# Kernel tuning notes

Measured on AMD Instinct MI355X. Metric: run time of the kernel, lower is better.

Reference implementation:

```python
import jax, jax.numpy as jnp
import numpy as np

N_NODES, N_EDGES = 10000, 160000
LATENT, N_EXP, N_SPECIES = 128, 8, 16
AVG_NEIGH = 16.0
EPS = 1e-8
# irreps: 64x0e + 32x1e + 16x2e -> flat dim 64 + 32*3 + 16*5 = 240

def _split(x):
    return x[:, :64], x[:, 64:160].reshape(-1, 32, 3), x[:, 160:240].reshape(-1, 16, 5)

def _merge(s, v, t):
    return jnp.concatenate([s, v.reshape(v.shape[0], -1), t.reshape(t.shape[0], -1)], axis=-1)

def _sep_ln(x, g, b):
    # separable layer norm: LN on scalars, per-degree component RMS norm on l>0
    s, v, t = _split(x)
    s = (s - s.mean(-1, keepdims=True)) * jax.lax.rsqrt(s.var(-1, keepdims=True) + EPS) * g[:64] + b
    v = v * jax.lax.rsqrt((v * v).mean((1, 2), keepdims=True) + EPS) * g[64:96][None, :, None]
    t = t * jax.lax.rsqrt((t * t).mean((1, 2), keepdims=True) + EPS) * g[96:112][None, :, None]
    return _merge(s, v, t)

def _forward(latents, node_features, edge_features, node_onehot, edge_vector,
             ln_gn, ln_bn, ln_ge, ln_be, Wg, W0, W1, W2, P0, b0, P1, P2,
             Wenv, benv, T0, T1, T2, edge_index):
    ec, en = edge_index[0], edge_index[1]
    nf_n = _sep_ln(node_features, ln_gn, ln_bn)
    ef_n = _sep_ln(edge_features, ln_ge, ln_be)
    # gather center/neighbor node features per edge (irregular access)
    c0, c1, c2 = _split(nf_n[ec])
    n0, n1, n2 = _split(nf_n[en])
    e0, e1, e2 = _split(ef_n)
    in0 = jnp.concatenate([c0, e0, n0], -1)   # [E,192]
    in1 = jnp.concatenate([c1, e1, n1], 1)    # [E,96,3]
    in2 = jnp.concatenate([c2, e2, n2], 1)    # [E,48,5]
    # latent-conditioned MoE tensor product: per-l linear with expert-mixed weights
    gates = jax.nn.softmax(latents @ Wg, axis=-1)            # [E,K]
    out0 = jnp.einsum('ek,kio,ei->eo', gates, W0, in0)        # [E,112]
    out1 = jnp.einsum('ek,kio,eim->eom', gates, W1, in1)      # [E,32,3]
    out2 = jnp.einsum('ek,kio,eim->eom', gates, W2, in2)      # [E,16,5]
    # gated nonlinearity: silu scalars, sigmoid gates multiply l>0 blocks
    s = jax.nn.silu(out0[:, :64])
    g1 = jax.nn.sigmoid(out0[:, 64:96])
    g2 = jax.nn.sigmoid(out0[:, 96:112])
    v = out1 * g1[:, :, None]
    t = out2 * g2[:, :, None]
    # lin_post (per-degree linear, bias on scalars)
    s = s @ P0 + b0
    v = jnp.einsum('eim,io->eom', v, P1)
    t = jnp.einsum('eim,io->eom', t, P2)
    # env element-wise weighting from latents (E3ElementLinear)
    w = latents @ Wenv + benv                                 # [E,112]
    msg = _merge(s * w[:, :64], v * w[:, 64:96, None], t * w[:, 96:112, None])
    # scatter-aggregate to center nodes
    agg = jax.ops.segment_sum(msg, ec, num_segments=node_features.shape[0])
    new_nf = agg * (AVG_NEIGH ** -0.5)
    # residual update with logit-parametrized ratio (param=0 -> u=0.5)
    u = jax.nn.sigmoid(jnp.zeros((), new_nf.dtype))
    c_old = jax.lax.rsqrt(u * u + 1.0)
    c_new = u * c_old
    nf = c_old * node_features + c_new * new_nf
    # species one-hot fully-connected TP correction
    s2, v2, t2 = _split(nf)
    ds = jnp.einsum('ni,nk,iko->no', s2, node_onehot, T0)
    dv = jnp.einsum('nim,nk,iko->nom', v2, node_onehot, T1)
    dt = jnp.einsum('nim,nk,iko->nom', t2, node_onehot, T2)
    return nf + _merge(ds, dv, dt)

def setup_inputs():
    key = jax.random.key(0)
    ks = jax.random.split(key, 20)
    f32 = jnp.float32
    return {
        'latents': jax.random.normal(ks[0], (N_EDGES, LATENT), f32),
        'node_features': jax.random.normal(ks[1], (N_NODES, 240), f32),
        'edge_features': jax.random.normal(ks[2], (N_EDGES, 240), f32),
        'node_onehot': jax.nn.one_hot(jax.random.randint(ks[3], (N_NODES,), 0, N_SPECIES), N_SPECIES, dtype=f32),
        'edge_vector': jax.random.normal(ks[4], (N_EDGES, 3), f32),
        'ln_gn': jnp.ones((112,), f32), 'ln_bn': jnp.zeros((64,), f32),
        'ln_ge': jnp.ones((112,), f32), 'ln_be': jnp.zeros((64,), f32),
        'Wg': jax.random.normal(ks[5], (LATENT, N_EXP), f32) * 0.1,
        'W0': jax.random.normal(ks[6], (N_EXP, 192, 112), f32) / float(np.sqrt(192)),
        'W1': jax.random.normal(ks[7], (N_EXP, 96, 32), f32) / float(np.sqrt(96)),
        'W2': jax.random.normal(ks[8], (N_EXP, 48, 16), f32) / float(np.sqrt(48)),
        'P0': jax.random.normal(ks[9], (64, 64), f32) / 8.0,
        'b0': jnp.zeros((64,), f32),
        'P1': jax.random.normal(ks[10], (32, 32), f32) / float(np.sqrt(32)),
        'P2': jax.random.normal(ks[11], (16, 16), f32) / 4.0,
        'Wenv': jax.random.normal(ks[12], (LATENT, 112), f32) / float(np.sqrt(LATENT)),
        'benv': jnp.zeros((112,), f32),
        'T0': jax.random.normal(ks[13], (64, N_SPECIES, 64), f32) / float(np.sqrt(64 * N_SPECIES)),
        'T1': jax.random.normal(ks[14], (32, N_SPECIES, 32), f32) / float(np.sqrt(32 * N_SPECIES)),
        'T2': jax.random.normal(ks[15], (16, N_SPECIES, 16), f32) / float(np.sqrt(16 * N_SPECIES)),
        'edge_index': jax.random.randint(ks[16], (2, N_EDGES), 0, N_NODES),
    }

def reference(latents, node_features, edge_features, node_onehot, edge_vector,
              ln_gn, ln_bn, ln_ge, ln_be, Wg, W0, W1, W2, P0, b0, P1, P2,
              Wenv, benv, T0, T1, T2, edge_index):
    return _forward(latents, node_features, edge_features, node_onehot, edge_vector,
                    ln_gn, ln_bn, ln_ge, ln_be, Wg, W0, W1, W2, P0, b0, P1, P2,
                    Wenv, benv, T0, T1, T2, edge_index)
```

## Files before the change

kernel.cpp:

```cpp
#include <hip/hip_runtime.h>
#include <math.h>

#define N_NODES 10000
#define N_EDGES 160000
#define EPS 1e-8f

typedef __attribute__((ext_vector_type(8))) __bf16 bf16x8;
typedef __attribute__((ext_vector_type(4))) float f32x4;

__device__ __forceinline__ f32x4 MFMA(bf16x8 a, bf16x8 b, f32x4 c){
  return __builtin_amdgcn_mfma_f32_16x16x32_bf16(a, b, c, 0, 0, 0);
}

__device__ __forceinline__ float wave_sum64(float x) {
  #pragma unroll
  for (int m = 32; m >= 1; m >>= 1) x += __shfl_xor(x, m, 64);
  return x;
}
__device__ __forceinline__ float gsum16(float x) {
  x += __shfl_xor(x, 1, 64); x += __shfl_xor(x, 2, 64);
  x += __shfl_xor(x, 4, 64); x += __shfl_xor(x, 8, 64);
  return x;
}

#define X0O 0
#define X1O 6400
#define X2O 16384
#define WvO 27904
#define O0O 0
#define O1O 6400
#define O2O 16384
#define SMEM_BYTES 64640

#define W0O 0
#define W1O 196608
#define W2O 221184
#define WEO 229376
#define P0O 245760
#define P1O 249856
#define P2O 250880
#define WTOT 251392

__device__ __forceinline__ void prep_seg(int u, const float* __restrict__ src,
                                         __bf16* __restrict__ dst,
                                         int NT, int KS, int Ka, int Na) {
  int per = NT * KS * 512;
  int e = u / per; int r = u - e * per;
  int nt = r / (KS * 512); r -= nt * KS * 512;
  int ks = r >> 9; int li = r & 511;
  int lane = li >> 3, j = li & 7;
  int k = ks * 32 + ((lane >> 4) << 3) + j;
  int n = nt * 16 + (lane & 15);
  float v = (k < Ka && n < Na) ? src[((size_t)e * Ka + k) * Na + n] : 0.f;
  dst[u] = (__bf16)v;
}

__global__ __launch_bounds__(256)
void k_prep(const float* __restrict__ W0, const float* __restrict__ W1,
            const float* __restrict__ W2, const float* __restrict__ We,
            const float* __restrict__ P0, const float* __restrict__ P1,
            const float* __restrict__ P2, __bf16* __restrict__ dst) {
  int t = blockIdx.x * 256 + threadIdx.x;
  if (t >= WTOT) return;
  if      (t < W1O) prep_seg(t - W0O, W0, dst + W0O, 8, 6, 192, 112);
  else if (t < W2O) prep_seg(t - W1O, W1, dst + W1O, 2, 3,  96,  32);
  else if (t < WEO) prep_seg(t - W2O, W2, dst + W2O, 1, 2,  48,  16);
  else if (t < P0O) prep_seg(t - WEO, We, dst + WEO, 8, 4, 128, 112);
  else if (t < P1O) prep_seg(t - P0O, P0, dst + P0O, 4, 2,  64,  64);
  else if (t < P2O) prep_seg(t - P1O, P1, dst + P1O, 2, 1,  32,  32);
  else              prep_seg(t - P2O, P2, dst + P2O, 1, 1,  16,  16);
}

__global__ __launch_bounds__(256)
void k_node_ln(const float* __restrict__ nf, const float* __restrict__ gn,
               const float* __restrict__ bn, __bf16* __restrict__ nfn) {
  int node = blockIdx.x * 4 + (threadIdx.x >> 6);
  int lane = threadIdx.x & 63;
  const float* row = nf + (size_t)node * 240;
  __bf16* out = nfn + (size_t)node * 240;
  float s = row[lane];
  float mean = wave_sum64(s) * (1.f / 64.f);
  float d = s - mean;
  float var = wave_sum64(d * d) * (1.f / 64.f);
  float rstd = rsqrtf(var + EPS);
  out[lane] = (__bf16)(d * rstd * gn[lane] + bn[lane]);
  float v0 = row[64 + lane];
  float v1 = (lane < 32) ? row[128 + lane] : 0.f;
  float rsv = rsqrtf(wave_sum64(v0 * v0 + v1 * v1) * (1.f / 96.f) + EPS);
  { int vi = lane; int i = vi / 3, m = vi - 3 * i;
    out[64 + m * 32 + i] = (__bf16)(v0 * rsv * gn[64 + i]); }
  if (lane < 32) { int vi = 64 + lane; int i = vi / 3, m = vi - 3 * i;
    out[64 + m * 32 + i] = (__bf16)(v1 * rsv * gn[64 + i]); }
  float t0 = row[160 + lane];
  float t1 = (lane < 16) ? row[224 + lane] : 0.f;
  float rst = rsqrtf(wave_sum64(t0 * t0 + t1 * t1) * (1.f / 80.f) + EPS);
  { int ti = lane; int i = ti / 5, m = ti - 5 * i;
    out[160 + m * 16 + i] = (__bf16)(t0 * rst * gn[96 + i]); }
  if (lane < 16) { int ti = 64 + lane; int i = ti / 5, m = ti - 5 * i;
    out[160 + m * 16 + i] = (__bf16)(t1 * rst * gn[96 + i]); }
}

__global__ __launch_bounds__(512, 4)
void k_edge(const float* __restrict__ latents, const float* __restrict__ ef,
            const __bf16* __restrict__ nfn, const int* __restrict__ eidx,
            const float* __restrict__ ln_ge, const float* __restrict__ ln_be,
            const float* __restrict__ Wg, const __bf16* __restrict__ Wsw,
            const float* __restrict__ pb0, const float* __restrict__ benv,
            float* __restrict__ agg) {
  __shared__ __align__(16) char smem[SMEM_BYTES];
  __bf16* SB = (__bf16*)smem;
  float* gatesL = (float*)(smem + 63488);
  int* ecsL = (int*)(smem + 64512);

  const int tid = threadIdx.x;
  const int e0 = blockIdx.x * 32;
  const int w = tid >> 6, lane = tid & 63, kg = lane >> 4, l16 = lane & 15;
  const int eg = tid >> 4, sl = tid & 15;

  const int ec = eidx[e0 + eg], en = eidx[N_EDGES + e0 + eg];
  if (tid < 32) ecsL[tid] = eidx[e0 + tid];
  uint2 cvr[4], nvr[4];
  #pragma unroll
  for (int j = 0; j < 4; ++j) {
    int ch = j * 16 + sl;
    if (ch < 60) {
      int p = ch * 4;
      cvr[j] = *(const uint2*)(nfn + (size_t)ec * 240 + p);
      nvr[j] = *(const uint2*)(nfn + (size_t)en * 240 + p);
    }
  }

  {
    const int mt = w >> 2, np = (w & 3) * 2;
    f32x4 acc[2] = {};
    const __bf16* WB = Wsw + WEO;
    #pragma unroll
    for (int ks = 0; ks < 4; ++ks) {
      bf16x8 a;
      const float* lp = latents + (size_t)(e0 + mt * 16 + l16) * 128 + ks * 32 + kg * 8;
      float4 u4 = *(const float4*)lp; float4 v4 = *(const float4*)(lp + 4);
      a[0]=(__bf16)u4.x; a[1]=(__bf16)u4.y; a[2]=(__bf16)u4.z; a[3]=(__bf16)u4.w;
      a[4]=(__bf16)v4.x; a[5]=(__bf16)v4.y; a[6]=(__bf16)v4.z; a[7]=(__bf16)v4.w;
      bf16x8 bA = *(const bf16x8*)(WB + ((np * 4 + ks) << 9) + lane * 8);
      bf16x8 bB = *(const bf16x8*)(WB + (((np + 1) * 4 + ks) << 9) + lane * 8);
      acc[0] = MFMA(a, bA, acc[0]); acc[1] = MFMA(a, bB, acc[1]);
    }
    #pragma unroll
    for (int ni = 0; ni < 2; ++ni) {
      int cc = (np + ni) * 16 + l16;
      if (cc < 112) {
        float bv = benv[cc];
        #pragma unroll
        for (int jj = 0; jj < 4; ++jj)
          SB[WvO + (mt * 16 + kg * 4 + jj) * 120 + cc] = (__bf16)(acc[ni][jj] + bv);
      }
    }
  }

  {
    #pragma unroll
    for (int j = 0; j < 4; ++j) {
      int ch = j * 16 + sl;
      if (ch < 60) {
        int p = ch * 4, dst, eoff;
        if (p < 64)       { dst = X0O + eg * 200 + p; eoff = 64; }
        else if (p < 160) { int q = p - 64; int m = q >> 5, i = q & 31;
                            dst = X1O + (m * 32 + eg) * 104 + i; eoff = 32; }
        else              { int q = p - 160; int m = q >> 4, i = q & 15;
                            dst = X2O + (m * 32 + eg) * 72 + i; eoff = 16; }
        *(uint2*)(SB + dst) = cvr[j];
        *(uint2*)(SB + dst + 2 * eoff) = nvr[j];
      }
    }
    for (int z = tid; z < 160 * 4; z += 512) {
      uint2 zz; zz.x = 0; zz.y = 0;
      *(uint2*)(SB + X2O + (z >> 2) * 72 + 48 + (z & 3) * 4) = zz;
    }

    const float* erow = ef + (size_t)(e0 + eg) * 240;
    float ev[15];
    #pragma unroll
    for (int j = 0; j < 15; ++j) ev[j] = erow[j * 16 + sl];
    float ssum = 0.f;
    #pragma unroll
    for (int j = 0; j < 4; ++j) ssum += ev[j];
    float mean = gsum16(ssum) * (1.f / 64.f);
    float sv = 0.f;
    #pragma unroll
    for (int j = 0; j < 4; ++j) { float dd = ev[j] - mean; sv += dd * dd; }
    float rstd = rsqrtf(gsum16(sv) * (1.f / 64.f) + EPS);
    float v2 = 0.f;
    #pragma unroll
    for (int j = 4; j < 10; ++j) v2 += ev[j] * ev[j];
    float rsv = rsqrtf(gsum16(v2) * (1.f / 96.f) + EPS);
    float t2 = 0.f;
    #pragma unroll
    for (int j = 10; j < 15; ++j) t2 += ev[j] * ev[j];
    float rst = rsqrtf(gsum16(t2) * (1.f / 80.f) + EPS);
    #pragma unroll
    for (int j = 0; j < 15; ++j) {
      const int c = j * 16 + sl;
      float x = ev[j], y; int eo;
      if (j < 4)       { y = (x - mean) * rstd * ln_ge[c] + ln_be[c];
                         eo = X0O + eg * 200 + 64 + c; }
      else if (j < 10) { int cc = c - 64; int i = cc / 3, m = cc - 3 * i;
                         y = x * rsv * ln_ge[64 + i];
                         eo = X1O + (m * 32 + eg) * 104 + 32 + i; }
      else             { int cc = c - 160; int i = cc / 5, m = cc - 5 * i;
                         y = x * rst * ln_ge[96 + i];
                         eo = X2O + (m * 32 + eg) * 72 + 16 + i; }
      SB[eo] = (__bf16)y;
    }

    const float* lrow = latents + (size_t)(e0 + eg) * 128 + sl * 8;
    float4 u4 = *(const float4*)lrow;
    float4 w4 = *(const float4*)(lrow + 4);
    float lv[8] = {u4.x, u4.y, u4.z, u4.w, w4.x, w4.y, w4.z, w4.w};
    float ga[8] = {};
    #pragma unroll
    for (int dd = 0; dd < 8; ++dd) {
      const float* wgr = Wg + (sl * 8 + dd) * 8;
      #pragma unroll
      for (int k = 0; k < 8; ++k) ga[k] += lv[dd] * wgr[k];
    }
    #pragma unroll
    for (int k = 0; k < 8; ++k) ga[k] = gsum16(ga[k]);
    float mx = ga[0];
    #pragma unroll
    for (int k = 1; k < 8; ++k) mx = fmaxf(mx, ga[k]);
    float den = 0.f;
    #pragma unroll
    for (int k = 0; k < 8; ++k) { ga[k] = expf(ga[k] - mx); den += ga[k]; }
    float val = 0.f;
    #pragma unroll
    for (int k = 0; k < 8; ++k) if (sl == k) val = ga[k];
    if (sl < 8) gatesL[eg * 8 + sl] = val / den;
  }
  __syncthreads();

  {
    const int mt = w & 1, ntA = (w >> 1) * 2;
    f32x4 acc[2] = {};
    const __bf16* WB = Wsw + W0O;
    for (int ex = 0; ex < 8; ++ex) {
      f32x4 D[2] = {};
      #pragma unroll
      for (int ks = 0; ks < 6; ++ks) {
        bf16x8 a = *(const bf16x8*)(SB + X0O + (mt * 16 + l16) * 200 + ks * 32 + kg * 8);
        bf16x8 bA = *(const bf16x8*)(WB + (((ex * 8 + ntA) * 6 + ks) << 9) + lane * 8);
        bf16x8 bB = *(const bf16x8*)(WB + (((ex * 8 + ntA + 1) * 6 + ks) << 9) + lane * 8);
        D[0] = MFMA(a, bA, D[0]); D[1] = MFMA(a, bB, D[1]);
      }
      #pragma unroll
      for (int jj = 0; jj < 4; ++jj) {
        float g = gatesL[(mt * 16 + kg * 4 + jj) * 8 + ex];
        acc[0][jj] += g * D[0][jj]; acc[1][jj] += g * D[1][jj];
      }
    }
    __syncthreads();
    #pragma unroll
    for (int ni = 0; ni < 2; ++ni) {
      int cc = (ntA + ni) * 16 + l16;
      if (cc < 112)
        #pragma unroll
        for (int jj = 0; jj < 4; ++jj) {
          float x = acc[ni][jj];
          float sg = 1.f / (1.f + expf(-x));
          float val = (cc < 64) ? x * sg : sg;
          SB[O0O + (mt * 16 + kg * 4 + jj) * 120 + cc] = (__bf16)val;
        }
    }
  }

  const int nu1 = (w < 4) ? 2 : 1;
  const int mtv0 = w >> 1, ntv = w & 1, mtv1 = (w >> 1) + 4;
  {
    f32x4 acc[2] = {};
    const __bf16* WB = Wsw + W1O;
    for (int ex = 0; ex < 8; ++ex) {
      f32x4 D[2] = {};
      #pragma unroll
      for (int ks = 0; ks < 3; ++ks) {
        bf16x8 b = *(const bf16x8*)(WB + (((ex * 2 + ntv) * 3 + ks) << 9) + lane * 8);
        bf16x8 a0 = *(const bf16x8*)(SB + X1O + (mtv0 * 16 + l16) * 104 + ks * 32 + kg * 8);
        D[0] = MFMA(a0, b, D[0]);
        if (nu1 == 2) {
          bf16x8 a1 = *(const bf16x8*)(SB + X1O + (mtv1 * 16 + l16) * 104 + ks * 32 + kg * 8);
          D[1] = MFMA(a1, b, D[1]);
        }
      }
      #pragma unroll
      for (int jj = 0; jj < 4; ++jj) {
        int r0 = mtv0 * 16 + kg * 4 + jj;
        acc[0][jj] += gatesL[(r0 & 31) * 8 + ex] * D[0][jj];
        if (nu1 == 2) {
          int r1 = mtv1 * 16 + kg * 4 + jj;
          acc[1][jj] += gatesL[(r1 & 31) * 8 + ex] * D[1][jj];
        }
      }
    }
    __syncthreads();
    const int o = ntv * 16 + l16;
    #pragma unroll
    for (int jj = 0; jj < 4; ++jj) {
      int r0 = mtv0 * 16 + kg * 4 + jj;
      float g0 = (float)SB[O0O + (r0 & 31) * 120 + 64 + o];
      SB[O1O + r0 * 40 + o] = (__bf16)(acc[0][jj] * g0);
      if (nu1 == 2) {
        int r1 = mtv1 * 16 + kg * 4 + jj;
        float g1 = (float)SB[O0O + (r1 & 31) * 120 + 64 + o];
        SB[O1O + r1 * 40 + o] = (__bf16)(acc[1][jj] * g1);
      }
    }
  }

  const int nu2 = (w < 2) ? 2 : 1;
  const int mt20 = w, mt21 = w + 8;
  {
    f32x4 acc[2] = {};
    const __bf16* WB = Wsw + W2O;
    for (int ex = 0; ex < 8; ++ex) {
      f32x4 D[2] = {};
      #pragma unroll
      for (int ks = 0; ks < 2; ++ks) {
        bf16x8 b = *(const bf16x8*)(WB + ((ex * 2 + ks) << 9) + lane * 8);
        bf16x8 a0 = *(const bf16x8*)(SB + X2O + (mt20 * 16 + l16) * 72 + ks * 32 + kg * 8);
        D[0] = MFMA(a0, b, D[0]);
        if (nu2 == 2) {
          bf16x8 a1 = *(const bf16x8*)(SB + X2O + (mt21 * 16 + l16) * 72 + ks * 32 + kg * 8);
          D[1] = MFMA(a1, b, D[1]);
        }
      }
      #pragma unroll
      for (int jj = 0; jj < 4; ++jj) {
        int r0 = mt20 * 16 + kg * 4 + jj;
        acc[0][jj] += gatesL[(r0 & 31) * 8 + ex] * D[0][jj];
        if (nu2 == 2) {
          int r1 = mt21 * 16 + kg * 4 + jj;
          acc[1][jj] += gatesL[(r1 & 31) * 8 + ex] * D[1][jj];
        }
      }
    }
    __syncthreads();
    #pragma unroll
    for (int jj = 0; jj < 4; ++jj) {
      int r0 = mt20 * 16 + kg * 4 + jj;
      float g0 = (float)SB[O0O + (r0 & 31) * 120 + 96 + l16];
      SB[O2O + r0 * 40 + l16] = (__bf16)(acc[0][jj] * g0);
      SB[O2O + r0 * 40 + 16 + l16] = (__bf16)0.f;
      if (nu2 == 2) {
        int r1 = mt21 * 16 + kg * 4 + jj;
        float g1 = (float)SB[O0O + (r1 & 31) * 120 + 96 + l16];
        SB[O2O + r1 * 40 + l16] = (__bf16)(acc[1][jj] * g1);
        SB[O2O + r1 * 40 + 16 + l16] = (__bf16)0.f;
      }
    }
  }
  __syncthreads();

  {
    const int mt = w & 1, nt = w >> 1;
    f32x4 ps = {};
    const __bf16* WB = Wsw + P0O;
    #pragma unroll
    for (int ks = 0; ks < 2; ++ks) {
      bf16x8 a = *(const bf16x8*)(SB + O0O + (mt * 16 + l16) * 120 + ks * 32 + kg * 8);
      bf16x8 b = *(const bf16x8*)(WB + ((nt * 2 + ks) << 9) + lane * 8);
      ps = MFMA(a, b, ps);
    }
    int cc = nt * 16 + l16;
    float bias = pb0[cc];
    #pragma unroll
    for (int jj = 0; jj < 4; ++jj) {
      int row = mt * 16 + kg * 4 + jj;
      float msg = (ps[jj] + bias) * (float)SB[WvO + row * 120 + cc];
      atomicAdd(&agg[(size_t)ecsL[row] * 240 + cc], msg);
    }
  }
  {
    f32x4 pv[2] = {};
    const __bf16* WB = Wsw + P1O;
    bf16x8 b = *(const bf16x8*)(WB + (ntv << 9) + lane * 8);
    bf16x8 a0 = *(const bf16x8*)(SB + O1O + (mtv0 * 16 + l16) * 40 + kg * 8);
    pv[0] = MFMA(a0, b, pv[0]);
    if (nu1 == 2) {
      bf16x8 a1 = *(const bf16x8*)(SB + O1O + (mtv1 * 16 + l16) * 40 + kg * 8);
      pv[1] = MFMA(a1, b, pv[1]);
    }
    const int o = ntv * 16 + l16;
    #pragma unroll
    for (int jj = 0; jj < 4; ++jj) {
      int r0 = mtv0 * 16 + kg * 4 + jj;
      int m = r0 >> 5, eL = r0 & 31;
      float msg = pv[0][jj] * (float)SB[WvO + eL * 120 + 64 + o];
      atomicAdd(&agg[(size_t)ecsL[eL] * 240 + 64 + m * 32 + o], msg);
      if (nu1 == 2) {
        int r1 = mtv1 * 16 + kg * 4 + jj;
        int m1 = r1 >> 5, eL1 = r1 & 31;
        float msg1 = pv[1][jj] * (float)SB[WvO + eL1 * 120 + 64 + o];
        atomicAdd(&agg[(size_t)ecsL[eL1] * 240 + 64 + m1 * 32 + o], msg1);
      }
    }
  }
  {
    f32x4 pt[2] = {};
    const __bf16* WB = Wsw + P2O;
    bf16x8 b = *(const bf16x8*)(WB + lane * 8);
    bf16x8 a0 = *(const bf16x8*)(SB + O2O + (mt20 * 16 + l16) * 40 + kg * 8);
    pt[0] = MFMA(a0, b, pt[0]);
    if (nu2 == 2) {
      bf16x8 a1 = *(const bf16x8*)(SB + O2O + (mt21 * 16 + l16) * 40 + kg * 8);
      pt[1] = MFMA(a1, b, pt[1]);
    }
    const int o = l16;
    #pragma unroll
    for (int jj = 0; jj < 4; ++jj) {
      int r0 = mt20 * 16 + kg * 4 + jj;
      int m = r0 >> 5, eL = r0 & 31;
      float msg = pt[0][jj] * (float)SB[WvO + eL * 120 + 96 + o];
      atomicAdd(&agg[(size_t)ecsL[eL] * 240 + 160 + m * 16 + o], msg);
      if (nu2 == 2) {
        int r1 = mt21 * 16 + kg * 4 + jj;
        int m1 = r1 >> 5, eL1 = r1 & 31;
        float msg1 = pt[1][jj] * (float)SB[WvO + eL1 * 120 + 96 + o];
        atomicAdd(&agg[(size_t)ecsL[eL1] * 240 + 160 + m1 * 16 + o], msg1);
      }
    }
  }
}

__global__ __launch_bounds__(256)
void k_node(const float* __restrict__ nf, const float* __restrict__ agg,
            const float* __restrict__ onehot, const float* __restrict__ T0,
            const float* __restrict__ T1, const float* __restrict__ T2,
            float* __restrict__ out) {
  int w = threadIdx.x >> 6;
  int lane = threadIdx.x & 63;
  int node = blockIdx.x * 4 + w;
  __shared__ float buf[4][240];
  const float* nrow = nf + (size_t)node * 240;
  const float* arow = agg + (size_t)node * 240;
  const float c_old = 0.894427190999916f;
  const float c_new_s = 0.447213595499958f * 0.25f;
  for (int j = lane; j < 240; j += 64) {
    int src;
    if (j < 64) src = j;
    else if (j < 160) { int vi = j - 64; int o = vi / 3, m = vi - 3 * o; src = 64 + m * 32 + o; }
    else              { int ti = j - 160; int o = ti / 5, m = ti - 5 * o; src = 160 + m * 16 + o; }
    buf[w][j] = c_old * nrow[j] + c_new_s * arow[src];
  }
  float ohv = (lane < 16) ? onehot[(size_t)node * 16 + lane] : 0.f;
  unsigned long long msk = __ballot(ohv > 0.5f);
  int kk = __ffsll((unsigned long long)msk) - 1;
  __syncthreads();
  #pragma unroll
  for (int rep = 0; rep < 4; ++rep) {
    int c = rep * 64 + lane;
    if (c >= 240) break;
    float d;
    if (c < 64) {
      const float* tp = T0 + (size_t)kk * 64 + c;
      float a = 0.f;
      for (int i = 0; i < 64; ++i) a = fmaf(buf[w][i], tp[(size_t)i * 1024], a);
      d = a;
    } else if (c < 160) {
      int vi = c - 64; int o = vi / 3, m = vi - o * 3;
      const float* tp = T1 + (size_t)kk * 32 + o;
      float a = 0.f;
      for (int i = 0; i < 32; ++i) a = fmaf(buf[w][64 + i * 3 + m], tp[(size_t)i * 512], a);
      d = a;
    } else {
      int ti = c - 160; int o = ti / 5, m = ti - o * 5;
      const float* tp = T2 + (size_t)kk * 16 + o;
      float a = 0.f;
      for (int i = 0; i < 16; ++i) a = fmaf(buf[w][160 + i * 5 + m], tp[(size_t)i * 256], a);
      d = a;
    }
    out[(size_t)node * 240 + c] = buf[w][c] + d;
  }
}

extern "C" void kernel_launch(void* const* d_in, const int* in_sizes, int n_in,
                              void* d_out, int out_size, void* d_ws, size_t ws_size,
                              hipStream_t stream) {
  (void)in_sizes; (void)n_in; (void)out_size; (void)ws_size;
  const float* latents       = (const float*)d_in[0];
  const float* node_features = (const float*)d_in[1];
  const float* edge_features = (const float*)d_in[2];
  const float* node_onehot   = (const float*)d_in[3];
  const float* ln_gn = (const float*)d_in[5];
  const float* ln_bn = (const float*)d_in[6];
  const float* ln_ge = (const float*)d_in[7];
  const float* ln_be = (const float*)d_in[8];
  const float* Wg    = (const float*)d_in[9];
  const float* W0    = (const float*)d_in[10];
  const float* W1    = (const float*)d_in[11];
  const float* W2    = (const float*)d_in[12];
  const float* P0    = (const float*)d_in[13];
  const float* b0    = (const float*)d_in[14];
  const float* P1    = (const float*)d_in[15];
  const float* P2    = (const float*)d_in[16];
  const float* Wenv  = (const float*)d_in[17];
  const float* benv  = (const float*)d_in[18];
  const float* T0    = (const float*)d_in[19];
  const float* T1    = (const float*)d_in[20];
  const float* T2    = (const float*)d_in[21];
  const int*   eidx  = (const int*)d_in[22];
  float* out = (float*)d_out;

  __bf16* nfn = (__bf16*)d_ws;
  float* agg = (float*)((char*)d_ws + 4800000);
  __bf16* Wsw = (__bf16*)((char*)d_ws + 14400000);

  hipMemsetAsync(agg, 0, 2400000 * sizeof(float), stream);
  k_prep<<<(WTOT + 255) / 256, 256, 0, stream>>>(W0, W1, W2, Wenv, P0, P1, P2, Wsw);
  k_node_ln<<<N_NODES / 4, 256, 0, stream>>>(node_features, ln_gn, ln_bn, nfn);
  k_edge<<<N_EDGES / 32, 512, 0, stream>>>(latents, edge_features, nfn, eidx,
      ln_ge, ln_be, Wg, Wsw, b0, benv, agg);
  k_node<<<N_NODES / 4, 256, 0, stream>>>(node_features, agg, node_onehot, T0, T1, T2, out);
}
```

Measured before the change: 436.9 us.

## Split edge LN stats and gating into pre-kernels, shrink and swizzle edge LDS

```diff
diff --git a/kernel.cpp b/kernel.cpp
--- a/kernel.cpp
+++ b/kernel.cpp
@@ -24,13 +24,13 @@
 }
 
 #define X0O 0
-#define X1O 6400
-#define X2O 16384
-#define WvO 27904
+#define X1O 6144
+#define X2O 15360
 #define O0O 0
-#define O1O 6400
-#define O2O 16384
-#define SMEM_BYTES 64640
+#define O1O 6144
+#define O2O 15360
+#define WvO 21760
+#define SMEM_BYTES 52352
 
 #define W0O 0
 #define W1O 196608
@@ -100,26 +100,79 @@
     out[160 + m * 16 + i] = (__bf16)(t1 * rst * gn[96 + i]); }
 }
 
-__global__ __launch_bounds__(512, 4)
+__global__ __launch_bounds__(256)
+void k_stats(const float* __restrict__ ef, float4* __restrict__ stats) {
+  int row = blockIdx.x * 4 + (threadIdx.x >> 6);
+  int lane = threadIdx.x & 63;
+  const float* r = ef + (size_t)row * 240;
+  float s = r[lane];
+  float mean = wave_sum64(s) * (1.f / 64.f);
+  float d = s - mean;
+  float var = wave_sum64(d * d) * (1.f / 64.f);
+  float rstd = rsqrtf(var + EPS);
+  float v0 = r[64 + lane];
+  float v1 = (lane < 32) ? r[128 + lane] : 0.f;
+  float rsv = rsqrtf(wave_sum64(v0 * v0 + v1 * v1) * (1.f / 96.f) + EPS);
+  float t0 = r[160 + lane];
+  float t1 = (lane < 16) ? r[224 + lane] : 0.f;
+  float rst = rsqrtf(wave_sum64(t0 * t0 + t1 * t1) * (1.f / 80.f) + EPS);
+  if (lane == 0) stats[row] = make_float4(mean, rstd, rsv, rst);
+}
+
+__global__ __launch_bounds__(256)
+void k_gate(const float* __restrict__ latents, const float* __restrict__ Wg,
+            float* __restrict__ gatesG) {
+  int row = blockIdx.x * 16 + (threadIdx.x >> 4);
+  int sl = threadIdx.x & 15;
+  const float* lrow = latents + (size_t)row * 128 + sl * 8;
+  float4 u4 = *(const float4*)lrow;
+  float4 w4 = *(const float4*)(lrow + 4);
+  float lv[8] = {u4.x, u4.y, u4.z, u4.w, w4.x, w4.y, w4.z, w4.w};
+  float ga[8] = {};
+  #pragma unroll
+  for (int dd = 0; dd < 8; ++dd) {
+    const float* wgr = Wg + (sl * 8 + dd) * 8;
+    #pragma unroll
+    for (int k = 0; k < 8; ++k) ga[k] += lv[dd] * wgr[k];
+  }
+  #pragma unroll
+  for (int k = 0; k < 8; ++k) ga[k] = gsum16(ga[k]);
+  float mx = ga[0];
+  #pragma unroll
+  for (int k = 1; k < 8; ++k) mx = fmaxf(mx, ga[k]);
+  float den = 0.f;
+  #pragma unroll
+  for (int k = 0; k < 8; ++k) { ga[k] = expf(ga[k] - mx); den += ga[k]; }
+  float val = 0.f;
+  #pragma unroll
+  for (int k = 0; k < 8; ++k) if (sl == k) val = ga[k];
+  if (sl < 8) gatesG[(size_t)row * 8 + sl] = val / den;
+}
+
+__global__ __launch_bounds__(512, 6)
 void k_edge(const float* __restrict__ latents, const float* __restrict__ ef,
             const __bf16* __restrict__ nfn, const int* __restrict__ eidx,
             const float* __restrict__ ln_ge, const float* __restrict__ ln_be,
-            const float* __restrict__ Wg, const __bf16* __restrict__ Wsw,
+            const float4* __restrict__ stats, const float* __restrict__ gatesG,
+            const __bf16* __restrict__ Wsw,
             const float* __restrict__ pb0, const float* __restrict__ benv,
             float* __restrict__ agg) {
   __shared__ __align__(16) char smem[SMEM_BYTES];
-  __bf16* SB = (__bf16*)smem;
-  float* gatesL = (float*)(smem + 63488);
-  int* ecsL = (int*)(smem + 64512);
+  float* gatesL = (float*)(smem + 51200);
+  int* ecsL = (int*)(smem + 52224);
+  __bf16* SBF = (__bf16*)smem;
 
   const int tid = threadIdx.x;
   const int e0 = blockIdx.x * 32;
   const int w = tid >> 6, lane = tid & 63, kg = lane >> 4, l16 = lane & 15;
   const int eg = tid >> 4, sl = tid & 15;
+  const int xsw = (eg & 7) << 4;
+  const int xswr = (l16 & 7) << 4;
 
   const int ec = eidx[e0 + eg], en = eidx[N_EDGES + e0 + eg];
   if (tid < 32) ecsL[tid] = eidx[e0 + tid];
-  uint2 cvr[4], nvr[4];
+  if (tid < 256) gatesL[tid] = gatesG[(size_t)e0 * 8 + tid];
+  uint2 cvr[4], nvr[4]; float4 evf[4];
   #pragma unroll
   for (int j = 0; j < 4; ++j) {
     int ch = j * 16 + sl;
@@ -127,6 +180,180 @@
       int p = ch * 4;
       cvr[j] = *(const uint2*)(nfn + (size_t)ec * 240 + p);
       nvr[j] = *(const uint2*)(nfn + (size_t)en * 240 + p);
+      evf[j] = *(const float4*)(ef + (size_t)(e0 + eg) * 240 + p);
+    }
+  }
+  float4 st = stats[e0 + eg];
+
+  {
+    #pragma unroll
+    for (int j = 0; j < 4; ++j) {
+      int ch = j * 16 + sl;
+      if (ch < 60) {
+        int p = ch * 4;
+        float e4[4] = {evf[j].x, evf[j].y, evf[j].z, evf[j].w};
+        if (p < 64) {
+          int off = X0O + eg * 192;
+          *(uint2*)(smem + (((off + p) * 2) ^ xsw)) = cvr[j];
+          *(uint2*)(smem + (((off + 128 + p) * 2) ^ xsw)) = nvr[j];
+          __bf16 eb[4];
+          #pragma unroll
+          for (int t = 0; t < 4; ++t) {
+            int c = p + t;
+            eb[t] = (__bf16)((e4[t] - st.x) * st.y * ln_ge[c] + ln_be[c]);
+          }
+          *(uint2*)(smem + (((off + 64 + p) * 2) ^ xsw)) = *(uint2*)eb;
+        } else if (p < 160) {
+          int q = p - 64;
+          int m = q >> 5, i = q & 31;
+          int off = X1O + (m * 32 + eg) * 96;
+          *(uint2*)(smem + (((off + i) * 2) ^ xsw)) = cvr[j];
+          *(uint2*)(smem + (((off + 64 + i) * 2) ^ xsw)) = nvr[j];
+          #pragma unroll
+          for (int t = 0; t < 4; ++t) {
+            int k = q + t; int ei = k / 3, em = k - 3 * ei;
+            float y = e4[t] * st.z * ln_ge[64 + ei];
+            *(__bf16*)(smem + (((X1O + (em * 32 + eg) * 96 + 32 + ei) * 2) ^ xsw)) = (__bf16)y;
+          }
+        } else {
+          int q = p - 160;
+          int m = q >> 4, i = q & 15;
+          int off = X2O + (m * 32 + eg) * 64;
+          *(uint2*)(smem + (((off + i) * 2) ^ xsw)) = cvr[j];
+          *(uint2*)(smem + (((off + 32 + i) * 2) ^ xsw)) = nvr[j];
+          #pragma unroll
+          for (int t = 0; t < 4; ++t) {
+            int k = q + t; int ei = k / 5, em = k - 5 * ei;
+            float y = e4[t] * st.w * ln_ge[96 + ei];
+            *(__bf16*)(smem + (((X2O + (em * 32 + eg) * 64 + 16 + ei) * 2) ^ xsw)) = (__bf16)y;
+          }
+        }
+      }
+    }
+    for (int z = tid; z < 640; z += 512) {
+      int r = z >> 2, c4 = (z & 3) * 4;
+      uint2 zz; zz.x = 0; zz.y = 0;
+      *(uint2*)(smem + (((X2O + r * 64 + 48 + c4) * 2) ^ ((r & 7) << 4))) = zz;
+    }
+  }
+  __syncthreads();
+
+  {
+    const int mt = w & 1, ntA = (w >> 1) * 2;
+    f32x4 acc[2] = {};
+    const __bf16* WB = Wsw + W0O;
+    for (int ex = 0; ex < 8; ++ex) {
+      f32x4 D[2] = {};
+      #pragma unroll
+      for (int ks = 0; ks < 6; ++ks) {
+        bf16x8 a = *(const bf16x8*)(smem + (((X0O + (mt * 16 + l16) * 192 + ks * 32 + kg * 8) * 2) ^ xswr));
+        bf16x8 bA = *(const bf16x8*)(WB + (((ex * 8 + ntA) * 6 + ks) << 9) + lane * 8);
+        bf16x8 bB = *(const bf16x8*)(WB + (((ex * 8 + ntA + 1) * 6 + ks) << 9) + lane * 8);
+        D[0] = MFMA(a, bA, D[0]); D[1] = MFMA(a, bB, D[1]);
+      }
+      #pragma unroll
+      for (int jj = 0; jj < 4; ++jj) {
+        float g = gatesL[(mt * 16 + kg * 4 + jj) * 8 + ex];
+        acc[0][jj] += g * D[0][jj]; acc[1][jj] += g * D[1][jj];
+      }
+    }
+    __syncthreads();
+    #pragma unroll
+    for (int ni = 0; ni < 2; ++ni) {
+      int cc = (ntA + ni) * 16 + l16;
+      if (cc < 112)
+        #pragma unroll
+        for (int jj = 0; jj < 4; ++jj) {
+          float x = acc[ni][jj];
+          float sg = 1.f / (1.f + expf(-x));
+          float val = (cc < 64) ? x * sg : sg;
+          SBF[O0O + (mt * 16 + kg * 4 + jj) * 120 + cc] = (__bf16)val;
+        }
+    }
+  }
+
+  const int nu1 = (w < 4) ? 2 : 1;
+  const int mtv0 = w >> 1, ntv = w & 1, mtv1 = (w >> 1) + 4;
+  {
+    f32x4 acc[2] = {};
+    const __bf16* WB = Wsw + W1O;
+    for (int ex = 0; ex < 8; ++ex) {
+      f32x4 D[2] = {};
+      #pragma unroll
+      for (int ks = 0; ks < 3; ++ks) {
+        bf16x8 b = *(const bf16x8*)(WB + (((ex * 2 + ntv) * 3 + ks) << 9) + lane * 8);
+        bf16x8 a0 = *(const bf16x8*)(smem + (((X1O + (mtv0 * 16 + l16) * 96 + ks * 32 + kg * 8) * 2) ^ xswr));
+        D[0] = MFMA(a0, b, D[0]);
+        if (nu1 == 2) {
+          bf16x8 a1 = *(const bf16x8*)(smem + (((X1O + (mtv1 * 16 + l16) * 96 + ks * 32 + kg * 8) * 2) ^ xswr));
+          D[1] = MFMA(a1, b, D[1]);
+        }
+      }
+      #pragma unroll
+      for (int jj = 0; jj < 4; ++jj) {
+        int r0 = mtv0 * 16 + kg * 4 + jj;
+        acc[0][jj] += gatesL[(r0 & 31) * 8 + ex] * D[0][jj];
+        if (nu1 == 2) {
+          int r1 = mtv1 * 16 + kg * 4 + jj;
+          acc[1][jj] += gatesL[(r1 & 31) * 8 + ex] * D[1][jj];
+        }
+      }
+    }
+    __syncthreads();
+    const int o = ntv * 16 + l16;
+    #pragma unroll
+    for (int jj = 0; jj < 4; ++jj) {
+      int r0 = mtv0 * 16 + kg * 4 + jj;
+      float g0 = (float)SBF[O0O + (r0 & 31) * 120 + 64 + o];
+      SBF[O1O + r0 * 40 + o] = (__bf16)(acc[0][jj] * g0);
+      if (nu1 == 2) {
+        int r1 = mtv1 * 16 + kg * 4 + jj;
+        float g1 = (float)SBF[O0O + (r1 & 31) * 120 + 64 + o];
+        SBF[O1O + r1 * 40 + o] = (__bf16)(acc[1][jj] * g1);
+      }
+    }
+  }
+
+  const int nu2 = (w < 2) ? 2 : 1;
+  const int mt20 = w, mt21 = w + 8;
+  {
+    f32x4 acc[2] = {};
+    const __bf16* WB = Wsw + W2O;
+    for (int ex = 0; ex < 8; ++ex) {
+      f32x4 D[2] = {};
+      #pragma unroll
+      for (int ks = 0; ks < 2; ++ks) {
+        bf16x8 b = *(const bf16x8*)(WB + ((ex * 2 + ks) << 9) + lane * 8);
+        bf16x8 a0 = *(const bf16x8*)(smem + (((X2O + (mt20 * 16 + l16) * 64 + ks * 32 + kg * 8) * 2) ^ xswr));
+        D[0] = MFMA(a0, b, D[0]);
+        if (nu2 == 2) {
+          bf16x8 a1 = *(const bf16x8*)(smem + (((X2O + (mt21 * 16 + l16) * 64 + ks * 32 + kg * 8) * 2) ^ xswr));
+          D[1] = MFMA(a1, b, D[1]);
+        }
+      }
+      #pragma unroll
+      for (int jj = 0; jj < 4; ++jj) {
+        int r0 = mt20 * 16 + kg * 4 + jj;
+        acc[0][jj] += gatesL[(r0 & 31) * 8 + ex] * D[0][jj];
+        if (nu2 == 2) {
+          int r1 = mt21 * 16 + kg * 4 + jj;
+          acc[1][jj] += gatesL[(r1 & 31) * 8 + ex] * D[1][jj];
+        }
+      }
+    }
+    __syncthreads();
+    #pragma unroll
+    for (int jj = 0; jj < 4; ++jj) {
+      int r0 = mt20 * 16 + kg * 4 + jj;
+      float g0 = (float)SBF[O0O + (r0 & 31) * 120 + 96 + l16];
+      SBF[O2O + r0 * 40 + l16] = (__bf16)(acc[0][jj] * g0);
+      SBF[O2O + r0 * 40 + 16 + l16] = (__bf16)0.f;
+      if (nu2 == 2) {
+        int r1 = mt21 * 16 + kg * 4 + jj;
+        float g1 = (float)SBF[O0O + (r1 & 31) * 120 + 96 + l16];
+        SBF[O2O + r1 * 40 + l16] = (__bf16)(acc[1][jj] * g1);
+        SBF[O2O + r1 * 40 + 16 + l16] = (__bf16)0.f;
+      }
     }
   }
 
@@ -152,207 +379,7 @@
         float bv = benv[cc];
         #pragma unroll
         for (int jj = 0; jj < 4; ++jj)
-          SB[WvO + (mt * 16 + kg * 4 + jj) * 120 + cc] = (__bf16)(acc[ni][jj] + bv);
-      }
-    }
-  }
-
-  {
-    #pragma unroll
-    for (int j = 0; j < 4; ++j) {
-      int ch = j * 16 + sl;
-      if (ch < 60) {
-        int p = ch * 4, dst, eoff;
-        if (p < 64)       { dst = X0O + eg * 200 + p; eoff = 64; }
-        else if (p < 160) { int q = p - 64; int m = q >> 5, i = q & 31;
-                            dst = X1O + (m * 32 + eg) * 104 + i; eoff = 32; }
-        else              { int q = p - 160; int m = q >> 4, i = q & 15;
-                            dst = X2O + (m * 32 + eg) * 72 + i; eoff = 16; }
-        *(uint2*)(SB + dst) = cvr[j];
-        *(uint2*)(SB + dst + 2 * eoff) = nvr[j];
-      }
-    }
-    for (int z = tid; z < 160 * 4; z += 512) {
-      uint2 zz; zz.x = 0; zz.y = 0;
-      *(uint2*)(SB + X2O + (z >> 2) * 72 + 48 + (z & 3) * 4) = zz;
-    }
-
-    const float* erow = ef + (size_t)(e0 + eg) * 240;
-    float ev[15];
-    #pragma unroll
-    for (int j = 0; j < 15; ++j) ev[j] = erow[j * 16 + sl];
-    float ssum = 0.f;
-    #pragma unroll
-    for (int j = 0; j < 4; ++j) ssum += ev[j];
-    float mean = gsum16(ssum) * (1.f / 64.f);
-    float sv = 0.f;
-    #pragma unroll
-    for (int j = 0; j < 4; ++j) { float dd = ev[j] - mean; sv += dd * dd; }
-    float rstd = rsqrtf(gsum16(sv) * (1.f / 64.f) + EPS);
-    float v2 = 0.f;
-    #pragma unroll
-    for (int j = 4; j < 10; ++j) v2 += ev[j] * ev[j];
-    float rsv = rsqrtf(gsum16(v2) * (1.f / 96.f) + EPS);
-    float t2 = 0.f;
-    #pragma unroll
-    for (int j = 10; j < 15; ++j) t2 += ev[j] * ev[j];
-    float rst = rsqrtf(gsum16(t2) * (1.f / 80.f) + EPS);
-    #pragma unroll
-    for (int j = 0; j < 15; ++j) {
-      const int c = j * 16 + sl;
-      float x = ev[j], y; int eo;
-      if (j < 4)       { y = (x - mean) * rstd * ln_ge[c] + ln_be[c];
-                         eo = X0O + eg * 200 + 64 + c; }
-      else if (j < 10) { int cc = c - 64; int i = cc / 3, m = cc - 3 * i;
-                         y = x * rsv * ln_ge[64 + i];
-                         eo = X1O + (m * 32 + eg) * 104 + 32 + i; }
-      else             { int cc = c - 160; int i = cc / 5, m = cc - 5 * i;
-                         y = x * rst * ln_ge[96 + i];
-                         eo = X2O + (m * 32 + eg) * 72 + 16 + i; }
-      SB[eo] = (__bf16)y;
-    }
-
-    const float* lrow = latents + (size_t)(e0 + eg) * 128 + sl * 8;
-    float4 u4 = *(const float4*)lrow;
-    float4 w4 = *(const float4*)(lrow + 4);
-    float lv[8] = {u4.x, u4.y, u4.z, u4.w, w4.x, w4.y, w4.z, w4.w};
-    float ga[8] = {};
-    #pragma unroll
-    for (int dd = 0; dd < 8; ++dd) {
-      const float* wgr = Wg + (sl * 8 + dd) * 8;
-      #pragma unroll
-      for (int k = 0; k < 8; ++k) ga[k] += lv[dd] * wgr[k];
-    }
-    #pragma unroll
-    for (int k = 0; k < 8; ++k) ga[k] = gsum16(ga[k]);
-    float mx = ga[0];
-    #pragma unroll
-    for (int k = 1; k < 8; ++k) mx = fmaxf(mx, ga[k]);
-    float den = 0.f;
-    #pragma unroll
-    for (int k = 0; k < 8; ++k) { ga[k] = expf(ga[k] - mx); den += ga[k]; }
-    float val = 0.f;
-    #pragma unroll
-    for (int k = 0; k < 8; ++k) if (sl == k) val = ga[k];
-    if (sl < 8) gatesL[eg * 8 + sl] = val / den;
-  }
-  __syncthreads();
-
-  {
-    const int mt = w & 1, ntA = (w >> 1) * 2;
-    f32x4 acc[2] = {};
-    const __bf16* WB = Wsw + W0O;
-    for (int ex = 0; ex < 8; ++ex) {
-      f32x4 D[2] = {};
-      #pragma unroll
-      for (int ks = 0; ks < 6; ++ks) {
-        bf16x8 a = *(const bf16x8*)(SB + X0O + (mt * 16 + l16) * 200 + ks * 32 + kg * 8);
-        bf16x8 bA = *(const bf16x8*)(WB + (((ex * 8 + ntA) * 6 + ks) << 9) + lane * 8);
-        bf16x8 bB = *(const bf16x8*)(WB + (((ex * 8 + ntA + 1) * 6 + ks) << 9) + lane * 8);
-        D[0] = MFMA(a, bA, D[0]); D[1] = MFMA(a, bB, D[1]);
-      }
-      #pragma unroll
-      for (int jj = 0; jj < 4; ++jj) {
-        float g = gatesL[(mt * 16 + kg * 4 + jj) * 8 + ex];
-        acc[0][jj] += g * D[0][jj]; acc[1][jj] += g * D[1][jj];
-      }
-    }
-    __syncthreads();
-    #pragma unroll
-    for (int ni = 0; ni < 2; ++ni) {
-      int cc = (ntA + ni) * 16 + l16;
-      if (cc < 112)
-        #pragma unroll
-        for (int jj = 0; jj < 4; ++jj) {
-          float x = acc[ni][jj];
-          float sg = 1.f / (1.f + expf(-x));
-          float val = (cc < 64) ? x * sg : sg;
-          SB[O0O + (mt * 16 + kg * 4 + jj) * 120 + cc] = (__bf16)val;
-        }
-    }
-  }
-
-  const int nu1 = (w < 4) ? 2 : 1;
-  const int mtv0 = w >> 1, ntv = w & 1, mtv1 = (w >> 1) + 4;
-  {
-    f32x4 acc[2] = {};
-    const __bf16* WB = Wsw + W1O;
-    for (int ex = 0; ex < 8; ++ex) {
-      f32x4 D[2] = {};
-      #pragma unroll
-      for (int ks = 0; ks < 3; ++ks) {
-        bf16x8 b = *(const bf16x8*)(WB + (((ex * 2 + ntv) * 3 + ks) << 9) + lane * 8);
-        bf16x8 a0 = *(const bf16x8*)(SB + X1O + (mtv0 * 16 + l16) * 104 + ks * 32 + kg * 8);
-        D[0] = MFMA(a0, b, D[0]);
-        if (nu1 == 2) {
-          bf16x8 a1 = *(const bf16x8*)(SB + X1O + (mtv1 * 16 + l16) * 104 + ks * 32 + kg * 8);
-          D[1] = MFMA(a1, b, D[1]);
-        }
-      }
-      #pragma unroll
-      for (int jj = 0; jj < 4; ++jj) {
-        int r0 = mtv0 * 16 + kg * 4 + jj;
-        acc[0][jj] += gatesL[(r0 & 31) * 8 + ex] * D[0][jj];
-        if (nu1 == 2) {
-          int r1 = mtv1 * 16 + kg * 4 + jj;
-          acc[1][jj] += gatesL[(r1 & 31) * 8 + ex] * D[1][jj];
-        }
-      }
-    }
-    __syncthreads();
-    const int o = ntv * 16 + l16;
-    #pragma unroll
-    for (int jj = 0; jj < 4; ++jj) {
-      int r0 = mtv0 * 16 + kg * 4 + jj;
-      float g0 = (float)SB[O0O + (r0 & 31) * 120 + 64 + o];
-      SB[O1O + r0 * 40 + o] = (__bf16)(acc[0][jj] * g0);
-      if (nu1 == 2) {
-        int r1 = mtv1 * 16 + kg * 4 + jj;
-        float g1 = (float)SB[O0O + (r1 & 31) * 120 + 64 + o];
-        SB[O1O + r1 * 40 + o] = (__bf16)(acc[1][jj] * g1);
-      }
-    }
-  }
-
-  const int nu2 = (w < 2) ? 2 : 1;
-  const int mt20 = w, mt21 = w + 8;
-  {
-    f32x4 acc[2] = {};
-    const __bf16* WB = Wsw + W2O;
-    for (int ex = 0; ex < 8; ++ex) {
-      f32x4 D[2] = {};
-      #pragma unroll
-      for (int ks = 0; ks < 2; ++ks) {
-        bf16x8 b = *(const bf16x8*)(WB + ((ex * 2 + ks) << 9) + lane * 8);
-        bf16x8 a0 = *(const bf16x8*)(SB + X2O + (mt20 * 16 + l16) * 72 + ks * 32 + kg * 8);
-        D[0] = MFMA(a0, b, D[0]);
-        if (nu2 == 2) {
-          bf16x8 a1 = *(const bf16x8*)(SB + X2O + (mt21 * 16 + l16) * 72 + ks * 32 + kg * 8);
-          D[1] = MFMA(a1, b, D[1]);
-        }
-      }
-      #pragma unroll
-      for (int jj = 0; jj < 4; ++jj) {
-        int r0 = mt20 * 16 + kg * 4 + jj;
-        acc[0][jj] += gatesL[(r0 & 31) * 8 + ex] * D[0][jj];
-        if (nu2 == 2) {
-          int r1 = mt21 * 16 + kg * 4 + jj;
-          acc[1][jj] += gatesL[(r1 & 31) * 8 + ex] * D[1][jj];
-        }
-      }
-    }
-    __syncthreads();
-    #pragma unroll
-    for (int jj = 0; jj < 4; ++jj) {
-      int r0 = mt20 * 16 + kg * 4 + jj;
-      float g0 = (float)SB[O0O + (r0 & 31) * 120 + 96 + l16];
-      SB[O2O + r0 * 40 + l16] = (__bf16)(acc[0][jj] * g0);
-      SB[O2O + r0 * 40 + 16 + l16] = (__bf16)0.f;
-      if (nu2 == 2) {
-        int r1 = mt21 * 16 + kg * 4 + jj;
-        float g1 = (float)SB[O0O + (r1 & 31) * 120 + 96 + l16];
-        SB[O2O + r1 * 40 + l16] = (__bf16)(acc[1][jj] * g1);
-        SB[O2O + r1 * 40 + 16 + l16] = (__bf16)0.f;
+          SBF[WvO + (mt * 16 + kg * 4 + jj) * 120 + cc] = (__bf16)(acc[ni][jj] + bv);
       }
     }
   }
@@ -364,7 +391,7 @@
     const __bf16* WB = Wsw + P0O;
     #pragma unroll
     for (int ks = 0; ks < 2; ++ks) {
-      bf16x8 a = *(const bf16x8*)(SB + O0O + (mt * 16 + l16) * 120 + ks * 32 + kg * 8);
+      bf16x8 a = *(const bf16x8*)(SBF + O0O + (mt * 16 + l16) * 120 + ks * 32 + kg * 8);
       bf16x8 b = *(const bf16x8*)(WB + ((nt * 2 + ks) << 9) + lane * 8);
       ps = MFMA(a, b, ps);
     }
@@ -373,7 +400,7 @@
     #pragma unroll
     for (int jj = 0; jj < 4; ++jj) {
       int row = mt * 16 + kg * 4 + jj;
-      float msg = (ps[jj] + bias) * (float)SB[WvO + row * 120 + cc];
+      float msg = (ps[jj] + bias) * (float)SBF[WvO + row * 120 + cc];
       atomicAdd(&agg[(size_t)ecsL[row] * 240 + cc], msg);
     }
   }
@@ -381,10 +408,10 @@
     f32x4 pv[2] = {};
     const __bf16* WB = Wsw + P1O;
     bf16x8 b = *(const bf16x8*)(WB + (ntv << 9) + lane * 8);
-    bf16x8 a0 = *(const bf16x8*)(SB + O1O + (mtv0 * 16 + l16) * 40 + kg * 8);
+    bf16x8 a0 = *(const bf16x8*)(SBF + O1O + (mtv0 * 16 + l16) * 40 + kg * 8);
     pv[0] = MFMA(a0, b, pv[0]);
     if (nu1 == 2) {
-      bf16x8 a1 = *(const bf16x8*)(SB + O1O + (mtv1 * 16 + l16) * 40 + kg * 8);
+      bf16x8 a1 = *(const bf16x8*)(SBF + O1O + (mtv1 * 16 + l16) * 40 + kg * 8);
       pv[1] = MFMA(a1, b, pv[1]);
     }
     const int o = ntv * 16 + l16;
@@ -392,12 +419,12 @@
     for (int jj = 0; jj < 4; ++jj) {
       int r0 = mtv0 * 16 + kg * 4 + jj;
       int m = r0 >> 5, eL = r0 & 31;
-      float msg = pv[0][jj] * (float)SB[WvO + eL * 120 + 64 + o];
+      float msg = pv[0][jj] * (float)SBF[WvO + eL * 120 + 64 + o];
       atomicAdd(&agg[(size_t)ecsL[eL] * 240 + 64 + m * 32 + o], msg);
       if (nu1 == 2) {
         int r1 = mtv1 * 16 + kg * 4 + jj;
         int m1 = r1 >> 5, eL1 = r1 & 31;
-        float msg1 = pv[1][jj] * (float)SB[WvO + eL1 * 120 + 64 + o];
+        float msg1 = pv[1][jj] * (float)SBF[WvO + eL1 * 120 + 64 + o];
         atomicAdd(&agg[(size_t)ecsL[eL1] * 240 + 64 + m1 * 32 + o], msg1);
       }
     }
@@ -406,10 +433,10 @@
     f32x4 pt[2] = {};
     const __bf16* WB = Wsw + P2O;
     bf16x8 b = *(const bf16x8*)(WB + lane * 8);
-    bf16x8 a0 = *(const bf16x8*)(SB + O2O + (mt20 * 16 + l16) * 40 + kg * 8);
+    bf16x8 a0 = *(const bf16x8*)(SBF + O2O + (mt20 * 16 + l16) * 40 + kg * 8);
     pt[0] = MFMA(a0, b, pt[0]);
     if (nu2 == 2) {
-      bf16x8 a1 = *(const bf16x8*)(SB + O2O + (mt21 * 16 + l16) * 40 + kg * 8);
+      bf16x8 a1 = *(const bf16x8*)(SBF + O2O + (mt21 * 16 + l16) * 40 + kg * 8);
       pt[1] = MFMA(a1, b, pt[1]);
     }
     const int o = l16;
@@ -417,12 +444,12 @@
     for (int jj = 0; jj < 4; ++jj) {
       int r0 = mt20 * 16 + kg * 4 + jj;
       int m = r0 >> 5, eL = r0 & 31;
-      float msg = pt[0][jj] * (float)SB[WvO + eL * 120 + 96 + o];
+      float msg = pt[0][jj] * (float)SBF[WvO + eL * 120 + 96 + o];
       atomicAdd(&agg[(size_t)ecsL[eL] * 240 + 160 + m * 16 + o], msg);
       if (nu2 == 2) {
         int r1 = mt21 * 16 + kg * 4 + jj;
         int m1 = r1 >> 5, eL1 = r1 & 31;
-        float msg1 = pt[1][jj] * (float)SB[WvO + eL1 * 120 + 96 + o];
+        float msg1 = pt[1][jj] * (float)SBF[WvO + eL1 * 120 + 96 + o];
         atomicAdd(&agg[(size_t)ecsL[eL1] * 240 + 160 + m1 * 16 + o], msg1);
       }
     }
@@ -508,14 +535,18 @@
   const int*   eidx  = (const int*)d_in[22];
   float* out = (float*)d_out;
 
-  __bf16* nfn = (__bf16*)d_ws;
-  float* agg = (float*)((char*)d_ws + 4800000);
-  __bf16* Wsw = (__bf16*)((char*)d_ws + 14400000);
+  __bf16* nfn    = (__bf16*)d_ws;
+  float*  agg    = (float*)((char*)d_ws + 4800000);
+  __bf16* Wsw    = (__bf16*)((char*)d_ws + 14400000);
+  float4* stats  = (float4*)((char*)d_ws + 15000000);
+  float*  gatesG = (float*)((char*)d_ws + 17600000);
 
   hipMemsetAsync(agg, 0, 2400000 * sizeof(float), stream);
   k_prep<<<(WTOT + 255) / 256, 256, 0, stream>>>(W0, W1, W2, Wenv, P0, P1, P2, Wsw);
   k_node_ln<<<N_NODES / 4, 256, 0, stream>>>(node_features, ln_gn, ln_bn, nfn);
+  k_stats<<<N_EDGES / 4, 256, 0, stream>>>(edge_features, stats);
+  k_gate<<<N_EDGES / 16, 256, 0, stream>>>(latents, Wg, gatesG);
   k_edge<<<N_EDGES / 32, 512, 0, stream>>>(latents, edge_features, nfn, eidx,
-      ln_ge, ln_be, Wg, Wsw, b0, benv, agg);
+      ln_ge, ln_be, stats, gatesG, Wsw, b0, benv, agg);
   k_node<<<N_NODES / 4, 256, 0, stream>>>(node_features, agg, node_onehot, T0, T1, T2, out);
 }
```

Measured after the change: 1.279 ms. +192.8%, slower.
